# Kernel tuning notes

Measured on AMD Instinct MI355X. Metric: run time of the kernel, lower is better.

The kernel has to match this reference:

```python
import jax, jax.numpy as jnp
import numpy as np

DIM = 1024
HEADS = 16
HEAD_DIM = DIM // HEADS
RANK = 16
ALPHA = 8.0
SCALING = ALPHA / RANK  # 0.5
SCALE = HEAD_DIM ** (-0.5)
B_, L_ = 2, 2048


def _proj_params(key, std=0.02):
    kW, kb, kA, kB = jax.random.split(key, 4)
    W = jax.random.normal(kW, (DIM, DIM), jnp.float32) * std   # [out, in]
    b = jax.random.normal(kb, (DIM,), jnp.float32) * std
    A = jax.random.normal(kA, (DIM, RANK), jnp.float32) * std  # [out, r]
    Bm = jax.random.normal(kB, (RANK, DIM), jnp.float32) * std # [r, in]
    return W, b, A, Bm


def setup_inputs() -> dict:
    key = jax.random.key(0)
    ks = jax.random.split(key, 6)
    x = jax.random.normal(ks[0], (B_, L_, DIM), jnp.float32)
    attn_bias = jax.random.normal(ks[1], (1, HEADS, L_, L_), jnp.float32) * 0.1
    inp = {"x": x, "attn_bias": attn_bias}
    for name, k in zip("qkvo", ks[2:6]):
        W, b, A, Bm = _proj_params(k)
        inp[f"W{name}"] = W
        inp[f"b{name}"] = b
        inp[f"A{name}"] = A
        inp[f"B{name}"] = Bm
    return inp


def _lora_linear(x, W, b, A, Bm):
    # y = x W^T + b + scaling * ((x @ A) @ B)   (matches torch LoRALinear)
    return x @ W.T + b + SCALING * ((x @ A) @ Bm)


def _split(x):
    B, L, D = x.shape
    return jnp.swapaxes(x.reshape(B, L, HEADS, HEAD_DIM), 1, 2)  # [B,H,L,hd]


def reference(x, attn_bias, Wq, bq, Aq, Bq, Wk, bk, Ak, Bk, Wv, bv, Av, Bv, Wo, bo, Ao, Bo):
    B, L, D = x.shape
    q = _split(_lora_linear(x, Wq, bq, Aq, Bq))
    k = _split(_lora_linear(x, Wk, bk, Ak, Bk))
    v = _split(_lora_linear(x, Wv, bv, Av, Bv))
    scores = jnp.einsum('bhld,bhmd->bhlm', q, k) * SCALE + attn_bias
    attn = jax.nn.softmax(scores, axis=-1)  # dropout p=0 -> identity
    out = jnp.einsum('bhlm,bhmd->bhld', attn, v)
    out = jnp.swapaxes(out, 1, 2).reshape(B, L, D)  # merge heads
    return _lora_linear(out, Wo, bo, Ao, Bo)
```

## Files before the change

kernel.cpp:

```cpp
#include <hip/hip_runtime.h>
#include <cstdint>

typedef __bf16 bf16;
typedef __bf16 bf16x8 __attribute__((ext_vector_type(8)));
typedef __bf16 bf16x4 __attribute__((ext_vector_type(4)));
typedef float  f32x4  __attribute__((ext_vector_type(4)));
typedef float  f32x16 __attribute__((ext_vector_type(16)));
typedef int    i32x4  __attribute__((ext_vector_type(4)));

#define DIM   1024
#define LSEQ  2048
#define NH    16
#define HD    64
#define NTOK  4096

#define AS1C(p) ((const __attribute__((address_space(1))) void*)(unsigned long long)(uintptr_t)(p))
#define AS3P(p) ((__attribute__((address_space(3))) void*)(unsigned int)(uintptr_t)(p))
#define SB0 __builtin_amdgcn_sched_barrier(0)

__device__ __forceinline__ f32x4 mfma16(bf16x8 a, bf16x8 b, f32x4 c) {
  return __builtin_amdgcn_mfma_f32_16x16x32_bf16(a, b, c, 0, 0, 0);
}
__device__ __forceinline__ f32x16 mfma32(bf16x8 a, bf16x8 b, f32x16 c) {
  return __builtin_amdgcn_mfma_f32_32x32x16_bf16(a, b, c, 0, 0, 0);
}
__device__ __forceinline__ int pk2(float a, float b) {
  unsigned short ua = __builtin_bit_cast(unsigned short, (bf16)a);
  unsigned short ub = __builtin_bit_cast(unsigned short, (bf16)b);
  return (int)ua | ((int)ub << 16);
}

__global__ __launch_bounds__(256) void k_cvt(const float* __restrict__ x,
                                             bf16* __restrict__ xb) {
  const int i = (blockIdx.x * 256 + threadIdx.x) * 4;
  const f32x4 v = *(const f32x4*)(x + i);
  bf16x4 o;
  o[0] = (bf16)v[0]; o[1] = (bf16)v[1]; o[2] = (bf16)v[2]; o[3] = (bf16)v[3];
  *(bf16x4*)(xb + i) = o;
}

struct WeffArgs {
  const float* W[4]; const float* A[4]; const float* B[4]; bf16* out[4];
};

__global__ __launch_bounds__(256) void k_weff(WeffArgs args) {
  const int o = blockIdx.x;
  const int z = blockIdx.y;
  const float* __restrict__ W  = args.W[z];
  const float* __restrict__ A  = args.A[z];
  const float* __restrict__ Bm = args.B[z];
  bf16* __restrict__ out = args.out[z];
  float Bo[16];
#pragma unroll
  for (int r = 0; r < 16; ++r) Bo[r] = Bm[r * DIM + o];
#pragma unroll
  for (int j = 0; j < 4; ++j) {
    const int d = j * 256 + (int)threadIdx.x;
    const float* Ar = A + (size_t)d * 16;
    float acc = 0.f;
#pragma unroll
    for (int r = 0; r < 16; ++r) acc += Ar[r] * Bo[r];
    out[(size_t)o * DIM + d] = (bf16)(W[(size_t)o * DIM + d] + 0.5f * acc);
  }
}

template <int NF, bool F32OUT>
__device__ __forceinline__ void gemm_body(const bf16* __restrict__ X,
                                          const bf16* __restrict__ W,
                                          const float* __restrict__ bias,
                                          void* __restrict__ out,
                                          float scale, int m0, int n0) {
  constexpr int BN = NF * 32;
  __shared__ __align__(16) bf16 As[128 * 32];
  __shared__ __align__(16) bf16 Bs[BN * 32];
  const int tid  = threadIdx.x;
  const int lane = tid & 63, w = tid >> 6;
  const int l15 = lane & 15, l4 = lane >> 4;
  const int wr = w >> 1, wc = w & 1;
  const int srow = w * 16 + (lane >> 2);
  const int scol = (lane & 3) * 8;

  f32x4 acc[4][NF] = {};
  const bf16* ag = X + (size_t)m0 * DIM;
  const bf16* bg = W + (size_t)n0 * DIM;

  for (int kt = 0; kt < DIM / 32; ++kt) {
    const int k0 = kt * 32;
#pragma unroll
    for (int j = 0; j < 2; ++j) {
      const int row = j * 64 + srow;
      __builtin_amdgcn_global_load_lds(AS1C(ag + (size_t)row * DIM + k0 + scol),
                                       AS3P(As + (j * 64 + w * 16) * 32), 16, 0, 0);
      if (j * 64 < BN)
        __builtin_amdgcn_global_load_lds(AS1C(bg + (size_t)row * DIM + k0 + scol),
                                         AS3P(Bs + (j * 64 + w * 16) * 32), 16, 0, 0);
    }
    __syncthreads();
    bf16x8 af[4], bfr[NF];
#pragma unroll
    for (int m = 0; m < 4; ++m)
      af[m] = *(const bf16x8*)(As + (wr * 64 + m * 16 + l15) * 32 + l4 * 8);
#pragma unroll
    for (int n = 0; n < NF; ++n)
      bfr[n] = *(const bf16x8*)(Bs + (wc * NF * 16 + n * 16 + l15) * 32 + l4 * 8);
#pragma unroll
    for (int m = 0; m < 4; ++m)
#pragma unroll
      for (int n = 0; n < NF; ++n)
        acc[m][n] = mfma16(af[m], bfr[n], acc[m][n]);
    __syncthreads();
  }

#pragma unroll
  for (int m = 0; m < 4; ++m) {
    const int r0 = m0 + wr * 64 + m * 16 + l4 * 4;
#pragma unroll
    for (int n = 0; n < NF; ++n) {
      const int c = n0 + wc * NF * 16 + n * 16 + l15;
      const float bc = bias[c];
#pragma unroll
      for (int t = 0; t < 4; ++t) {
        const float y = (acc[m][n][t] + bc) * scale;
        if constexpr (F32OUT)
          ((float*)out)[(size_t)(r0 + t) * DIM + c] = y;
        else
          ((bf16*)out)[(size_t)(r0 + t) * DIM + c] = (bf16)y;
      }
    }
  }
}

__global__ __launch_bounds__(256) void k_gemm_qkv(
    const bf16* __restrict__ xb, const bf16* __restrict__ weff,
    const float* __restrict__ bq, const float* __restrict__ bk,
    const float* __restrict__ bv,
    bf16* __restrict__ q, bf16* __restrict__ k, bf16* __restrict__ v) {
  const int z = blockIdx.z;
  const bf16* W = weff + (size_t)z * DIM * DIM;
  const float* bias = (z == 0) ? bq : (z == 1) ? bk : bv;
  bf16* out = (z == 0) ? q : (z == 1) ? k : v;
  const float scale = (z == 0) ? 0.125f : 1.0f;
  gemm_body<4, false>(xb, W, bias, out, scale, blockIdx.x * 128, blockIdx.y * 128);
}

__global__ __launch_bounds__(256) void k_gemm_o(
    const bf16* __restrict__ ctx, const bf16* __restrict__ weffo,
    const float* __restrict__ bo, float* __restrict__ out) {
  gemm_body<2, true>(ctx, weffo, bo, out, 1.0f, blockIdx.x * 128, blockIdx.y * 64);
}

__global__ __launch_bounds__(256) void k_vfrag(const bf16* __restrict__ v,
                                               const bf16* __restrict__ k,
                                               bf16* __restrict__ vf,
                                               bf16* __restrict__ kf) {
  const int lt = blockIdx.x, bh = blockIdx.y;
  const int b = bh >> 4, h = bh & 15;
  __shared__ __align__(16) bf16 tile[64][72];
  const int tid = threadIdx.x;
  const int r = tid >> 2, c0 = (tid & 3) * 16;
  const bf16* src = v + (size_t)(b * LSEQ + lt * 64) * DIM + h * HD;
  *(bf16x8*)(&tile[r][c0])     = *(const bf16x8*)(src + (size_t)r * DIM + c0);
  *(bf16x8*)(&tile[r][c0 + 8]) = *(const bf16x8*)(src + (size_t)r * DIM + c0 + 8);
  __syncthreads();
  const int w = tid >> 6, lane = tid & 63, l31 = lane & 31, hi = lane >> 5;
  {
    const int tt = w >> 1, n = w & 1;
    const int t = lt * 2 + tt;
#pragma unroll
    for (int c = 0; c < 2; ++c) {
      bf16 tmp[8];
#pragma unroll
      for (int j = 0; j < 8; ++j)
        tmp[j] = tile[tt * 32 + c * 16 + hi * 8 + j][n * 32 + l31];
      *(bf16x8*)(vf + ((((size_t)bh * 64 + t) * 4 + n * 2 + c) * 64 + lane) * 8) =
          *(bf16x8*)tmp;
    }
  }
  {
    const int t = lt * 2 + (w & 1);
    const bf16* krow = k + (size_t)(b * LSEQ + t * 32 + l31) * DIM + h * HD + hi * 8;
#pragma unroll
    for (int cc = 0; cc < 2; ++cc) {
      const int c = (w >> 1) + cc * 2;
      *(bf16x8*)(kf + ((((size_t)bh * 64 + t) * 4 + c) * 64 + lane) * 8) =
          *(const bf16x8*)(krow + c * 16);
    }
  }
}

__global__ __launch_bounds__(256, 2) void k_attn(
    const bf16* __restrict__ q, const bf16* __restrict__ kf,
    const bf16* __restrict__ vf, const float* __restrict__ bias,
    bf16* __restrict__ ctx) {
  const int tid = threadIdx.x, w = tid >> 6, lane = tid & 63;
  const int l31 = lane & 31, hi = lane >> 5;
  const int bh = blockIdx.x;
  const int b = bh >> 4, h = bh & 15;
  const int q0 = blockIdx.y * 128 + w * 32;

  __shared__ __align__(16) bf16  kls[3][2048];
  __shared__ __align__(16) bf16  vls[3][2048];
  __shared__ __align__(16) float bls[4][3][1024];

  const bf16* qrow = q + (size_t)(b * LSEQ + q0 + l31) * DIM + h * HD;
  bf16x8 Qf[4];
#pragma unroll
  for (int c = 0; c < 4; ++c) Qf[c] = *(const bf16x8*)(qrow + c * 16 + hi * 8);

  const bf16* kfb = kf + (size_t)bh * 64 * 2048 + w * 512 + lane * 8;
  const bf16* vfb = vf + (size_t)bh * 64 * 2048 + w * 512 + lane * 8;
  const int lr = lane >> 3, lc = lane & 7;
  const float* bsrc = bias + ((size_t)h * LSEQ + q0 + lr) * LSEQ + 4 * (lc ^ lr);

  f32x16 acc0 = {}, acc1 = {};
  float mrun = -3e38f, lrun = 0.f;

#define STAGE(ts_, s_)                                                         \
  {                                                                            \
    __builtin_amdgcn_global_load_lds(AS1C(kfb + (size_t)(ts_) * 2048),         \
                                     AS3P(&kls[s_][w * 512]), 16, 0, 0);       \
    __builtin_amdgcn_global_load_lds(AS1C(vfb + (size_t)(ts_) * 2048),         \
                                     AS3P(&vls[s_][w * 512]), 16, 0, 0);       \
    const float* bp_ = bsrc + (size_t)(ts_) * 32;                              \
    _Pragma("unroll") for (int g_ = 0; g_ < 4; ++g_)                           \
        __builtin_amdgcn_global_load_lds(AS1C(bp_ + (size_t)g_ * 8 * LSEQ),    \
                                         AS3P(&bls[w][s_][g_ * 256]), 16, 0, 0); \
  }

  STAGE(0, 0); SB0;
  STAGE(1, 1); SB0;

  int sl = 0, ss = 2;
  for (int t = 0; t < 64; ++t) {
    const int tn = (t + 2 > 63) ? 63 : t + 2;
    STAGE(tn, ss); SB0;
    asm volatile("s_waitcnt vmcnt(12)" ::: "memory");
    __builtin_amdgcn_s_barrier();

    bf16x8 Kf[4], Vf[2][2];
    f32x4 br[4];
#pragma unroll
    for (int c = 0; c < 4; ++c)
      Kf[c] = *(const bf16x8*)(&kls[sl][(c * 64 + lane) * 8]);
#pragma unroll
    for (int u = 0; u < 4; ++u)
      Vf[u >> 1][u & 1] = *(const bf16x8*)(&vls[sl][(u * 64 + lane) * 8]);
#pragma unroll
    for (int g = 0; g < 4; ++g)
      br[g] = *(const f32x4*)(
          &bls[w][sl][l31 * 32 + (((g << 3) | (hi << 2)) ^ ((l31 & 7) << 2))]);
    asm volatile("s_waitcnt lgkmcnt(0)" ::: "memory");
    SB0;
    __builtin_amdgcn_s_barrier();

    f32x16 s = {};
#pragma unroll
    for (int c = 0; c < 4; ++c) s = mfma32(Kf[c], Qf[c], s);
    float p[16];
#pragma unroll
    for (int r = 0; r < 16; ++r) p[r] = s[r] + br[r >> 2][r & 3];
    float m8[8];
#pragma unroll
    for (int i = 0; i < 8; ++i) m8[i] = fmaxf(p[i], p[i + 8]);
    float tm = fmaxf(fmaxf(fmaxf(m8[0], m8[4]), fmaxf(m8[1], m8[5])),
                     fmaxf(fmaxf(m8[2], m8[6]), fmaxf(m8[3], m8[7])));
    tm = fmaxf(tm, __shfl_xor(tm, 32));
    if (!__all(tm <= mrun + 8.0f)) {
      const float mn = fmaxf(mrun, tm);
      const float scl = __expf(mrun - mn);
      mrun = mn;
      lrun *= scl;
#pragma unroll
      for (int r = 0; r < 16; ++r) { acc0[r] *= scl; acc1[r] *= scl; }
    }
#pragma unroll
    for (int r = 0; r < 16; ++r) p[r] = __expf(p[r] - mrun);
    float s8[8];
#pragma unroll
    for (int i = 0; i < 8; ++i) s8[i] = p[i] + p[i + 8];
    float rs = ((s8[0] + s8[1]) + (s8[2] + s8[3])) + ((s8[4] + s8[5]) + (s8[6] + s8[7]));
    rs += __shfl_xor(rs, 32);
    lrun += rs;
#pragma unroll
    for (int c = 0; c < 2; ++c) {
      const int c8 = c * 8;
      const int A0 = pk2(p[c8 + 0], p[c8 + 1]);
      const int A1 = pk2(p[c8 + 2], p[c8 + 3]);
      const int B0 = pk2(p[c8 + 4], p[c8 + 5]);
      const int B1 = pk2(p[c8 + 6], p[c8 + 7]);
      const int pA0 = __shfl_xor(A0, 32), pA1 = __shfl_xor(A1, 32);
      const int pB0 = __shfl_xor(B0, 32), pB1 = __shfl_xor(B1, 32);
      i32x4 fi;
      fi[0] = hi ? pB0 : A0;
      fi[1] = hi ? pB1 : A1;
      fi[2] = hi ? B0 : pA0;
      fi[3] = hi ? B1 : pA1;
      const bf16x8 pf = __builtin_bit_cast(bf16x8, fi);
      acc0 = mfma32(Vf[0][c], pf, acc0);
      acc1 = mfma32(Vf[1][c], pf, acc1);
    }
    sl = (sl == 2) ? 0 : sl + 1;
    ss = (ss == 2) ? 0 : ss + 1;
  }
#undef STAGE

  const float inv = 1.0f / lrun;
  bf16* cp = ctx + (size_t)(b * LSEQ + q0 + l31) * DIM + h * HD;
#pragma unroll
  for (int r = 0; r < 16; ++r) {
    const int dr = (r & 3) + 8 * (r >> 2) + 4 * hi;
    cp[dr]      = (bf16)(acc0[r] * inv);
    cp[32 + dr] = (bf16)(acc1[r] * inv);
  }
}

extern "C" void kernel_launch(void* const* d_in, const int* in_sizes, int n_in,
                              void* d_out, int out_size, void* d_ws, size_t ws_size,
                              hipStream_t stream) {
  const float* x  = (const float*)d_in[0];
  const float* ab = (const float*)d_in[1];
  const float* Wq = (const float*)d_in[2];  const float* bq = (const float*)d_in[3];
  const float* Aq = (const float*)d_in[4];  const float* Bq = (const float*)d_in[5];
  const float* Wk = (const float*)d_in[6];  const float* bk = (const float*)d_in[7];
  const float* Ak = (const float*)d_in[8];  const float* Bk = (const float*)d_in[9];
  const float* Wv = (const float*)d_in[10]; const float* bv = (const float*)d_in[11];
  const float* Av = (const float*)d_in[12]; const float* Bv = (const float*)d_in[13];
  const float* Wo = (const float*)d_in[14]; const float* bo = (const float*)d_in[15];
  const float* Ao = (const float*)d_in[16]; const float* Bo = (const float*)d_in[17];

  uint8_t* ws = (uint8_t*)d_ws;
  const size_t SZ = (size_t)NTOK * DIM * sizeof(bf16);
  bf16* xb   = (bf16*)(ws + 0 * SZ);
  bf16* weff = (bf16*)(ws + 1 * SZ);
  bf16* qb   = (bf16*)(ws + 2 * SZ);
  bf16* kb   = (bf16*)(ws + 3 * SZ);
  bf16* vb   = (bf16*)(ws + 4 * SZ);
  bf16* kfb  = (bf16*)(ws + 5 * SZ);
  bf16* vfb  = (bf16*)(ws + 6 * SZ);
  bf16* ctx  = (bf16*)(ws + 7 * SZ);

  k_cvt<<<dim3(NTOK * DIM / 1024), 256, 0, stream>>>(x, xb);

  WeffArgs wa;
  wa.W[0] = Wq; wa.A[0] = Aq; wa.B[0] = Bq; wa.out[0] = weff;
  wa.W[1] = Wk; wa.A[1] = Ak; wa.B[1] = Bk; wa.out[1] = weff + (size_t)DIM * DIM;
  wa.W[2] = Wv; wa.A[2] = Av; wa.B[2] = Bv; wa.out[2] = weff + 2 * (size_t)DIM * DIM;
  wa.W[3] = Wo; wa.A[3] = Ao; wa.B[3] = Bo; wa.out[3] = weff + 3 * (size_t)DIM * DIM;
  k_weff<<<dim3(DIM, 4), 256, 0, stream>>>(wa);

  k_gemm_qkv<<<dim3(32, 8, 3), 256, 0, stream>>>(xb, weff, bq, bk, bv, qb, kb, vb);
  k_vfrag<<<dim3(32, 32), 256, 0, stream>>>(vb, kb, vfb, kfb);
  k_attn<<<dim3(32, 16), 256, 0, stream>>>(qb, kfb, vfb, ab, ctx);
  k_gemm_o<<<dim3(32, 16), 256, 0, stream>>>(ctx, weff + 3 * (size_t)DIM * DIM, bo,
                                             (float*)d_out);
}
```

Measured before the change: 183.4 us.

## Share attention bias tiles across batches by remapping waves to batch and query halves

Each attention block now covers one head and 64 query rows for both batch elements, with the four waves split as two batches times two 32-row query halves. The bias tile, which has no batch dimension, is staged once per block and read by both batch waves, halving bias traffic from global memory. The price is separate K/V LDS buffers per batch, which keeps total LDS about the same, and a smaller query tile per block.

New measurement: 183.2 us. About the same (-0.1%).

```diff
diff --git a/kernel.cpp b/kernel.cpp
--- a/kernel.cpp
+++ b/kernel.cpp
@@ -194,42 +194,50 @@
     bf16* __restrict__ ctx) {
   const int tid = threadIdx.x, w = tid >> 6, lane = tid & 63;
   const int l31 = lane & 31, hi = lane >> 5;
-  const int bh = blockIdx.x;
-  const int b = bh >> 4, h = bh & 15;
-  const int q0 = blockIdx.y * 128 + w * 32;
-
-  __shared__ __align__(16) bf16  kls[3][2048];
-  __shared__ __align__(16) bf16  vls[3][2048];
-  __shared__ __align__(16) float bls[4][3][1024];
-
-  const bf16* qrow = q + (size_t)(b * LSEQ + q0 + l31) * DIM + h * HD;
+  const int bb = w >> 1, qh = w & 1;
+  const int h = blockIdx.x & 15;
+  const int q0 = (blockIdx.x >> 4) * 64;
+
+  __shared__ __align__(16) bf16  kls[2][3][2048];
+  __shared__ __align__(16) bf16  vls[2][3][2048];
+  __shared__ __align__(16) float bls[2][3][1024];
+
+  const bf16* qrow = q + (size_t)(bb * LSEQ + q0 + qh * 32 + l31) * DIM + h * HD;
   bf16x8 Qf[4];
 #pragma unroll
   for (int c = 0; c < 4; ++c) Qf[c] = *(const bf16x8*)(qrow + c * 16 + hi * 8);
 
-  const bf16* kfb = kf + (size_t)bh * 64 * 2048 + w * 512 + lane * 8;
-  const bf16* vfb = vf + (size_t)bh * 64 * 2048 + w * 512 + lane * 8;
+  const int part2  = qh * 2;
+  const int bpart2 = bb * 2;
   const int lr = lane >> 3, lc = lane & 7;
-  const float* bsrc = bias + ((size_t)h * LSEQ + q0 + lr) * LSEQ + 4 * (lc ^ lr);
+  const bf16* ksrc = kf + (size_t)(bb * NH + h) * 64 * 2048 + part2 * 512 + lane * 8;
+  const bf16* vsrc = vf + (size_t)(bb * NH + h) * 64 * 2048 + part2 * 512 + lane * 8;
+  const float* bsrc =
+      bias + ((size_t)h * LSEQ + q0 + qh * 32 + bpart2 * 8 + lr) * LSEQ + 4 * (lc ^ lr);
 
   f32x16 acc0 = {}, acc1 = {};
   float mrun = -3e38f, lrun = 0.f;
 
-#define STAGE(ts_, s_)                                                         \
+#define STAGE(t_, s_)                                                          \
   {                                                                            \
-    __builtin_amdgcn_global_load_lds(AS1C(kfb + (size_t)(ts_) * 2048),         \
-                                     AS3P(&kls[s_][w * 512]), 16, 0, 0);       \
-    __builtin_amdgcn_global_load_lds(AS1C(vfb + (size_t)(ts_) * 2048),         \
-                                     AS3P(&vls[s_][w * 512]), 16, 0, 0);       \
-    const float* bp_ = bsrc + (size_t)(ts_) * 32;                              \
-    _Pragma("unroll") for (int g_ = 0; g_ < 4; ++g_)                           \
-        __builtin_amdgcn_global_load_lds(AS1C(bp_ + (size_t)g_ * 8 * LSEQ),    \
-                                         AS3P(&bls[w][s_][g_ * 256]), 16, 0, 0); \
+    __builtin_amdgcn_global_load_lds(AS1C(ksrc + (size_t)(t_) * 2048),         \
+                                     AS3P(&kls[bb][s_][part2 * 512]), 16, 0, 0);\
+    __builtin_amdgcn_global_load_lds(AS1C(ksrc + (size_t)(t_) * 2048 + 512),   \
+                                     AS3P(&kls[bb][s_][part2 * 512 + 512]), 16, 0, 0);\
+    __builtin_amdgcn_global_load_lds(AS1C(vsrc + (size_t)(t_) * 2048),         \
+                                     AS3P(&vls[bb][s_][part2 * 512]), 16, 0, 0);\
+    __builtin_amdgcn_global_load_lds(AS1C(vsrc + (size_t)(t_) * 2048 + 512),   \
+                                     AS3P(&vls[bb][s_][part2 * 512 + 512]), 16, 0, 0);\
+    __builtin_amdgcn_global_load_lds(AS1C(bsrc + (size_t)(t_) * 32),           \
+                                     AS3P(&bls[qh][s_][bpart2 * 256]), 16, 0, 0);\
+    __builtin_amdgcn_global_load_lds(AS1C(bsrc + (size_t)(t_) * 32 + 8 * LSEQ),\
+                                     AS3P(&bls[qh][s_][bpart2 * 256 + 256]), 16, 0, 0);\
   }
 
   STAGE(0, 0); SB0;
   STAGE(1, 1); SB0;
 
+  const int sw = (l31 & 7) << 2;
   int sl = 0, ss = 2;
   for (int t = 0; t < 64; ++t) {
     const int tn = (t + 2 > 63) ? 63 : t + 2;
@@ -241,14 +249,14 @@
     f32x4 br[4];
 #pragma unroll
     for (int c = 0; c < 4; ++c)
-      Kf[c] = *(const bf16x8*)(&kls[sl][(c * 64 + lane) * 8]);
+      Kf[c] = *(const bf16x8*)(&kls[bb][sl][c * 512 + lane * 8]);
 #pragma unroll
     for (int u = 0; u < 4; ++u)
-      Vf[u >> 1][u & 1] = *(const bf16x8*)(&vls[sl][(u * 64 + lane) * 8]);
+      Vf[u >> 1][u & 1] = *(const bf16x8*)(&vls[bb][sl][u * 512 + lane * 8]);
 #pragma unroll
     for (int g = 0; g < 4; ++g)
       br[g] = *(const f32x4*)(
-          &bls[w][sl][l31 * 32 + (((g << 3) | (hi << 2)) ^ ((l31 & 7) << 2))]);
+          &bls[qh][sl][l31 * 32 + (((g << 3) | (hi << 2)) ^ sw)]);
     asm volatile("s_waitcnt lgkmcnt(0)" ::: "memory");
     SB0;
     __builtin_amdgcn_s_barrier();
@@ -305,7 +313,7 @@
 #undef STAGE
 
   const float inv = 1.0f / lrun;
-  bf16* cp = ctx + (size_t)(b * LSEQ + q0 + l31) * DIM + h * HD;
+  bf16* cp = ctx + (size_t)(bb * LSEQ + q0 + qh * 32 + l31) * DIM + h * HD;
 #pragma unroll
   for (int r = 0; r < 16; ++r) {
     const int dr = (r & 3) + 8 * (r >> 2) + 4 * hi;
@@ -350,7 +358,7 @@
 
   k_gemm_qkv<<<dim3(32, 8, 3), 256, 0, stream>>>(xb, weff, bq, bk, bv, qb, kb, vb);
   k_vfrag<<<dim3(32, 32), 256, 0, stream>>>(vb, kb, vfb, kfb);
-  k_attn<<<dim3(32, 16), 256, 0, stream>>>(qb, kfb, vfb, ab, ctx);
+  k_attn<<<dim3(512), 256, 0, stream>>>(qb, kfb, vfb, ab, ctx);
   k_gemm_o<<<dim3(32, 16), 256, 0, stream>>>(ctx, weff + 3 * (size_t)DIM * DIM, bo,
                                              (float*)d_out);
 }
```
